# Optimization experiments

Measured on AMD Instinct MI355X. Metric: run time of the kernel, lower is better.

## Reference

```python
import jax, jax.numpy as jnp
import numpy as np

# Module hyperparameters (init_kwargs)
N_CODES = 1024    # context_size
Q_LEN = 8         # query_len
D_MODEL = 256     # d_model
BATCH = 16384
DECAY = 0.99
EPSILON = 1e-05


def setup_inputs() -> dict:
    key = jax.random.key(0)
    k1, k2, k3 = jax.random.split(key, 3)
    q = jax.random.normal(k1, (BATCH, Q_LEN, D_MODEL), jnp.float32)
    context = jax.random.normal(k2, (N_CODES, Q_LEN, D_MODEL), jnp.float32)
    ema_count = jnp.ones((N_CODES,), jnp.float32)
    ema_dw = jax.random.normal(k3, (N_CODES, Q_LEN, D_MODEL), jnp.float32) * 0.1
    return {"q": q, "context": context, "ema_count": ema_count, "ema_dw": ema_dw}


def _forward(q, context, ema_count, ema_dw):
    B, Q, D = q.shape
    N = context.shape[0]
    q_flat = q.reshape(B, Q * D)              # [B, QD]
    g_flat = context.reshape(N, Q * D)        # [N, QD]
    Dflat = Q * D

    # squared-euclidean cdist via the matmul expansion, then nearest code
    distances = (jnp.sum(q_flat * q_flat, axis=1, keepdims=True)
                 + jnp.sum(g_flat * g_flat, axis=1)
                 - 2.0 * (q_flat @ g_flat.T))                      # [B, N]
    indices = jnp.argmin(distances, axis=-1)                       # [B]

    # einsum('bn,nqd->bqd', one_hot, context) == gather
    q_context = context[indices]                                   # [B, Q, D]
    # einsum('bn,bqd->nqd', one_hot, q) == scatter-add by code id
    q_hat = jax.ops.segment_sum(q, indices, num_segments=N)        # [N, Q, D]

    # per-sample mean MSE (q_context detached in original)
    qld = jnp.mean((jax.lax.stop_gradient(q_context) - q) ** 2, axis=(1, 2))  # [B]

    # EMA codebook update (training mode, no-grad in original)
    counts = jax.ops.segment_sum(jnp.ones((B,), q.dtype), indices, num_segments=N)  # [N]
    ec = DECAY * ema_count + (1.0 - DECAY) * counts
    n = jnp.sum(ec)
    ec = (ec + EPSILON) / (n + Dflat * EPSILON) * n                # Laplace smoothing
    edw = DECAY * ema_dw + (1.0 - DECAY) * jax.lax.stop_gradient(q_hat)
    context_new = edw / ec[:, None, None]                          # [N, Q, D]

    # straight-through output uses the UPDATED (detached) context
    out_context = (q_hat + jax.lax.stop_gradient(context_new - q_hat)).reshape(-1, D)  # [N*Q, D]
    return qld, out_context, ec, edw, context_new


def reference(q, context, ema_count, ema_dw):
    return _forward(q, context, ema_count, ema_dw)
```

## Files before the change

kernel.cpp:

```cpp
#include <hip/hip_runtime.h>
#include <hip/hip_bf16.h>
#include <float.h>

#define BSZ 16384
#define NCODES 1024
#define QD 2048
#define NCHUNK 64
#define NCOLG 16

typedef _Float16 f16x8 __attribute__((ext_vector_type(8)));
typedef _Float16 f16x4 __attribute__((ext_vector_type(4)));
typedef float f32x4 __attribute__((ext_vector_type(4)));

static __device__ __forceinline__ float one_minus_decay() { return (float)(1.0 - 0.99); }

static __device__ __forceinline__ void async_copy16(const void* src, void* lds) {
    __builtin_amdgcn_global_load_lds((const __attribute__((address_space(1))) void*)src,
                                     (__attribute__((address_space(3))) void*)lds, 16, 0, 0);
}

__global__ void k_prep_all(const float* __restrict__ ctx, const float* __restrict__ q,
                           _Float16* __restrict__ gh, float* __restrict__ gsq,
                           _Float16* __restrict__ qh, float* __restrict__ qsq) {
    __shared__ float red[4];
    int tid = threadIdx.x;
    const float* src; _Float16* dh; float* nrm;
    if (blockIdx.x < NCODES) {
        size_t n = blockIdx.x;
        src = ctx + n * QD; dh = gh + n * QD; nrm = gsq + n;
    } else {
        size_t b = blockIdx.x - NCODES;
        src = q + b * QD; dh = qh + b * QD; nrm = qsq + b;
    }
    int c = tid * 8;
    float4 t0 = *(const float4*)(src + c);
    float4 t1 = *(const float4*)(src + c + 4);
    float s = t0.x * t0.x + t0.y * t0.y + t0.z * t0.z + t0.w * t0.w
            + t1.x * t1.x + t1.y * t1.y + t1.z * t1.z + t1.w * t1.w;
    f16x8 h;
    h[0] = (_Float16)t0.x; h[1] = (_Float16)t0.y;
    h[2] = (_Float16)t0.z; h[3] = (_Float16)t0.w;
    h[4] = (_Float16)t1.x; h[5] = (_Float16)t1.y;
    h[6] = (_Float16)t1.z; h[7] = (_Float16)t1.w;
    *(f16x8*)(dh + c) = h;
    for (int off = 32; off > 0; off >>= 1) s += __shfl_down(s, off);
    if ((tid & 63) == 0) red[tid >> 6] = s;
    __syncthreads();
    if (tid == 0) *nrm = red[0] + red[1] + red[2] + red[3];
}

__global__ void k_prep_r17(const float* __restrict__ ctx, const float* __restrict__ q,
                           _Float16* __restrict__ gh, float* __restrict__ gsq,
                           float* __restrict__ qsq) {
    int tid = threadIdx.x;
    if (blockIdx.x < NCODES) {
        __shared__ float red[4];
        int n = blockIdx.x;
        float s = 0.f;
#pragma unroll
        for (int i = 0; i < 2; ++i) {
            int c = (tid + i * 256) * 4;
            float4 t = *(const float4*)(ctx + (size_t)n * QD + c);
            f16x4 h;
            h[0] = (_Float16)t.x; h[1] = (_Float16)t.y;
            h[2] = (_Float16)t.z; h[3] = (_Float16)t.w;
            *(f16x4*)(gh + (size_t)n * QD + c) = h;
            s += t.x * t.x + t.y * t.y + t.z * t.z + t.w * t.w;
        }
        for (int off = 32; off > 0; off >>= 1) s += __shfl_down(s, off);
        if ((tid & 63) == 0) red[tid >> 6] = s;
        __syncthreads();
        if (tid == 0) gsq[n] = red[0] + red[1] + red[2] + red[3];
    } else {
        int w = tid >> 6, lane = tid & 63;
        int b = (blockIdx.x - NCODES) * 4 + w;
        const float4* row = (const float4*)(q + (size_t)b * QD);
        float s = 0.f;
#pragma unroll
        for (int i = 0; i < 8; ++i) {
            float4 v = row[lane + i * 64];
            s += v.x * v.x + v.y * v.y + v.z * v.z + v.w * v.w;
        }
        for (int off = 32; off > 0; off >>= 1) s += __shfl_down(s, off);
        if (lane == 0) qsq[b] = s;
    }
}

__launch_bounds__(256)
__global__ void k_dist_pre(const _Float16* __restrict__ qh, const _Float16* __restrict__ gh,
                           const float* __restrict__ gsq,
                           float* __restrict__ pval, int* __restrict__ pidx) {
    __shared__ _Float16 ah[128][64];
    __shared__ _Float16 bh[128][64];

    const int tid = threadIdx.x;
    const int lane = tid & 63, wid = tid >> 6;
    const int wr = wid >> 1, wc = wid & 1;
    const int n0 = blockIdx.x;
    const int xcd = n0 & 7, j = n0 >> 3;
    const int col = j & 7, rowt = xcd * 16 + (j >> 3);
    const int colBase = col * 128, rowBase = rowt * 128;
    const int fr = lane & 15, kg = lane >> 4;

    char* ahB = (char*)&ah[0][0];
    const char* bhB = (const char*)&bh[0][0];

    const int srow = lane >> 3;
    const int gran = (lane & 7) ^ (lane >> 3);

    f32x4 acc[4][4];
#pragma unroll
    for (int m = 0; m < 4; ++m)
#pragma unroll
        for (int n = 0; n < 4; ++n) acc[m][n] = (f32x4)0.f;

    for (int kb = 0; kb < QD; kb += 64) {
        __syncthreads();
#pragma unroll
        for (int i = 0; i < 4; ++i) {
            int g = wid * 4 + i;
            size_t aoff = (size_t)(rowBase + g * 8 + srow) * QD + kb + gran * 8;
            async_copy16(qh + aoff, &ah[g * 8][0]);
        }
#pragma unroll
        for (int i = 0; i < 4; ++i) {
            int g = wid * 4 + i;
            size_t goff = (size_t)(colBase + g * 8 + srow) * QD + kb + gran * 8;
            async_copy16(gh + goff, &bh[g * 8][0]);
        }
        __syncthreads();

#pragma unroll
        for (int h = 0; h < 2; ++h) {
            f16x8 a_h[4], b_h[4];
#pragma unroll
            for (int m = 0; m < 4; ++m) {
                int ar = wr * 64 + m * 16 + fr;
                int off = ar * 128 + ((h * 64 + kg * 16) ^ ((ar & 7) << 4));
                a_h[m] = *(const f16x8*)(ahB + off);
            }
#pragma unroll
            for (int n = 0; n < 4; ++n) {
                int br = wc * 64 + n * 16 + fr;
                int off = br * 128 + ((h * 64 + kg * 16) ^ ((br & 7) << 4));
                b_h[n] = *(const f16x8*)(bhB + off);
            }
#pragma unroll
            for (int m = 0; m < 4; ++m)
#pragma unroll
                for (int n = 0; n < 4; ++n)
                    acc[m][n] = __builtin_amdgcn_mfma_f32_16x16x32_f16(a_h[m], b_h[n], acc[m][n], 0, 0, 0);
        }
    }

    float mv[4][4]; int mi[4][4];
#pragma unroll
    for (int m = 0; m < 4; ++m)
#pragma unroll
        for (int r = 0; r < 4; ++r) { mv[m][r] = FLT_MAX; mi[m][r] = 0x7fffffff; }
#pragma unroll
    for (int n = 0; n < 4; ++n) {
        int c = colBase + wc * 64 + n * 16 + fr;
        float gq = gsq[c];
#pragma unroll
        for (int m = 0; m < 4; ++m)
#pragma unroll
            for (int r = 0; r < 4; ++r) {
                float d = gq - 2.0f * acc[m][n][r];
                if (d < mv[m][r]) { mv[m][r] = d; mi[m][r] = c; }
            }
    }
#pragma unroll
    for (int off = 1; off < 16; off <<= 1) {
#pragma unroll
        for (int m = 0; m < 4; ++m)
#pragma unroll
            for (int r = 0; r < 4; ++r) {
                float ov = __shfl_xor(mv[m][r], off);
                int   oi = __shfl_xor(mi[m][r], off);
                if (ov < mv[m][r] || (ov == mv[m][r] && oi < mi[m][r])) { mv[m][r] = ov; mi[m][r] = oi; }
            }
    }
    if (fr == 0) {
        const size_t slot = (size_t)(col * 2 + wc) * BSZ;
#pragma unroll
        for (int m = 0; m < 4; ++m)
#pragma unroll
            for (int r = 0; r < 4; ++r) {
                int grow = rowBase + wr * 64 + m * 16 + kg * 4 + r;
                pval[slot + grow] = mv[m][r];
                pidx[slot + grow] = mi[m][r];
            }
    }
}

__launch_bounds__(256)
__global__ void k_dist_r17(const float* __restrict__ q, const _Float16* __restrict__ gh,
                           const float* __restrict__ gsq,
                           float* __restrict__ pval, int* __restrict__ pidx) {
    __shared__ _Float16 ah[128][64];
    __shared__ _Float16 bh[128][64];

    const int tid = threadIdx.x;
    const int lane = tid & 63, wid = tid >> 6;
    const int wr = wid >> 1, wc = wid & 1;
    const int n0 = blockIdx.x;
    const int xcd = n0 & 7, j = n0 >> 3;
    const int col = j & 7, rowt = xcd * 16 + (j >> 3);
    const int colBase = col * 128, rowBase = rowt * 128;
    const int fr = lane & 15, kg = lane >> 4;

    char* ahB = (char*)&ah[0][0];
    const char* bhB = (const char*)&bh[0][0];

    f32x4 acc[4][4];
#pragma unroll
    for (int m = 0; m < 4; ++m)
#pragma unroll
        for (int n = 0; n < 4; ++n) acc[m][n] = (f32x4)0.f;

    for (int kb = 0; kb < QD; kb += 64) {
        __syncthreads();
#pragma unroll
        for (int s = 0; s < 8; ++s) {
            int f = s * 256 + tid;
            int row = f >> 4, k4 = (f & 15) * 4;
            float4 t = *(const float4*)(q + (size_t)(rowBase + row) * QD + kb + k4);
            f16x4 h;
            h[0] = (_Float16)t.x; h[1] = (_Float16)t.y;
            h[2] = (_Float16)t.z; h[3] = (_Float16)t.w;
            int byt = (row * 128 + k4 * 2) ^ ((row & 7) << 4);
            *(f16x4*)(ahB + byt) = h;
        }
#pragma unroll
        for (int i = 0; i < 4; ++i) {
            int g = wid * 4 + i;
            int row = g * 8 + (lane >> 3);
            int gran = (lane & 7) ^ (lane >> 3);
            size_t goff = (size_t)(colBase + row) * QD + kb + gran * 8;
            async_copy16(gh + goff, &bh[g * 8][0]);
        }
        __syncthreads();

#pragma unroll
        for (int h = 0; h < 2; ++h) {
            f16x8 a_h[4], b_h[4];
#pragma unroll
            for (int m = 0; m < 4; ++m) {
                int ar = wr * 64 + m * 16 + fr;
                int off = ar * 128 + ((h * 64 + kg * 16) ^ ((ar & 7) << 4));
                a_h[m] = *(const f16x8*)(ahB + off);
            }
#pragma unroll
            for (int n = 0; n < 4; ++n) {
                int br = wc * 64 + n * 16 + fr;
                int off = br * 128 + ((h * 64 + kg * 16) ^ ((br & 7) << 4));
                b_h[n] = *(const f16x8*)(bhB + off);
            }
#pragma unroll
            for (int m = 0; m < 4; ++m)
#pragma unroll
                for (int n = 0; n < 4; ++n)
                    acc[m][n] = __builtin_amdgcn_mfma_f32_16x16x32_f16(a_h[m], b_h[n], acc[m][n], 0, 0, 0);
        }
    }

    float mv[4][4]; int mi[4][4];
#pragma unroll
    for (int m = 0; m < 4; ++m)
#pragma unroll
        for (int r = 0; r < 4; ++r) { mv[m][r] = FLT_MAX; mi[m][r] = 0x7fffffff; }
#pragma unroll
    for (int n = 0; n < 4; ++n) {
        int c = colBase + wc * 64 + n * 16 + fr;
        float gq = gsq[c];
#pragma unroll
        for (int m = 0; m < 4; ++m)
#pragma unroll
            for (int r = 0; r < 4; ++r) {
                float d = gq - 2.0f * acc[m][n][r];
                if (d < mv[m][r]) { mv[m][r] = d; mi[m][r] = c; }
            }
    }
#pragma unroll
    for (int off = 1; off < 16; off <<= 1) {
#pragma unroll
        for (int m = 0; m < 4; ++m)
#pragma unroll
            for (int r = 0; r < 4; ++r) {
                float ov = __shfl_xor(mv[m][r], off);
                int   oi = __shfl_xor(mi[m][r], off);
                if (ov < mv[m][r] || (ov == mv[m][r] && oi < mi[m][r])) { mv[m][r] = ov; mi[m][r] = oi; }
            }
    }
    if (fr == 0) {
        const size_t slot = (size_t)(col * 2 + wc) * BSZ;
#pragma unroll
        for (int m = 0; m < 4; ++m)
#pragma unroll
            for (int r = 0; r < 4; ++r) {
                int grow = rowBase + wr * 64 + m * 16 + kg * 4 + r;
                pval[slot + grow] = mv[m][r];
                pidx[slot + grow] = mi[m][r];
            }
    }
}

__global__ void k_merge(const float* __restrict__ pval, const int* __restrict__ pidx,
                        const float* __restrict__ qsq,
                        int* __restrict__ idx_out, float* __restrict__ qld,
                        int* __restrict__ chunkhist) {
    __shared__ int h[NCODES];
    int c = blockIdx.x, tid = threadIdx.x;
    int b = c * 256 + tid;
#pragma unroll
    for (int s = 0; s < 4; ++s) h[tid + s * 256] = 0;
    float bv = pval[b]; int bi = pidx[b];
    for (int y = 1; y < NCOLG; ++y) {
        float v = pval[(size_t)y * BSZ + b]; int ii = pidx[(size_t)y * BSZ + b];
        if (v < bv || (v == bv && ii < bi)) { bv = v; bi = ii; }
    }
    idx_out[b] = bi;
    qld[b] = (qsq[b] + bv) * (1.0f / (float)QD);
    __syncthreads();
    atomicAdd(&h[bi], 1);
    __syncthreads();
#pragma unroll
    for (int s = 0; s < 4; ++s) chunkhist[c * NCODES + tid + s * 256] = h[tid + s * 256];
}

__global__ void k_scan(const int* __restrict__ chunkhist, int* __restrict__ base,
                       int* __restrict__ counts, int* __restrict__ offsets,
                       const float* __restrict__ ema_count, float* __restrict__ ec_out) {
    __shared__ int s[NCODES];
    __shared__ float e2[NCODES];
    int code = threadIdx.x;
    int run = 0;
    for (int c = 0; c < NCHUNK; ++c) {
        base[c * NCODES + code] = run;
        run += chunkhist[c * NCODES + code];
    }
    counts[code] = run;
    s[code] = run; __syncthreads();
    for (int off = 1; off < NCODES; off <<= 1) {
        int v = (code >= off) ? s[code - off] : 0;
        __syncthreads();
        s[code] += v; __syncthreads();
    }
    offsets[code] = s[code] - run;
    float er = 0.99f * ema_count[code] + one_minus_decay() * (float)run;
    e2[code] = er; __syncthreads();
    for (int off = 512; off > 0; off >>= 1) {
        if (code < off) e2[code] += e2[code + off];
        __syncthreads();
    }
    float n = e2[0];
    ec_out[code] = (er + 1e-5f) / (n + (float)(2048.0 * 1e-5)) * n;
}

__global__ void k_fill(const int* __restrict__ idx, const int* __restrict__ base,
                       const int* __restrict__ offsets, int* __restrict__ list) {
    __shared__ int sidx[256];
    int c = blockIdx.x, tid = threadIdx.x;
    int b = c * 256 + tid;
    int n = idx[b];
    sidx[tid] = n; __syncthreads();
    int rank = 0;
    for (int j = 0; j < tid; ++j) rank += (sidx[j] == n);
    list[offsets[n] + base[c * NCODES + n] + rank] = b;
}

__global__ void k_qhat(const float* __restrict__ q, const int* __restrict__ counts,
                       const int* __restrict__ offsets, const int* __restrict__ list,
                       float* __restrict__ qhat) {
    int n = blockIdx.x;
    int col = blockIdx.y * 256 + threadIdx.x;
    int cnt = counts[n];
    const int* lp = list + offsets[n];
    float a0 = 0.f, a1 = 0.f, a2 = 0.f, a3 = 0.f, a4 = 0.f, a5 = 0.f, a6 = 0.f, a7 = 0.f;
    int i = 0;
    for (; i + 8 <= cnt; i += 8) {
        int b0 = lp[i], b1 = lp[i + 1], b2 = lp[i + 2], b3 = lp[i + 3];
        int b4 = lp[i + 4], b5 = lp[i + 5], b6 = lp[i + 6], b7 = lp[i + 7];
        a0 += q[(size_t)b0 * QD + col]; a1 += q[(size_t)b1 * QD + col];
        a2 += q[(size_t)b2 * QD + col]; a3 += q[(size_t)b3 * QD + col];
        a4 += q[(size_t)b4 * QD + col]; a5 += q[(size_t)b5 * QD + col];
        a6 += q[(size_t)b6 * QD + col]; a7 += q[(size_t)b7 * QD + col];
    }
    for (; i < cnt; ++i) a0 += q[(size_t)lp[i] * QD + col];
    float r = ((a0 + a1) + (a2 + a3)) + ((a4 + a5) + (a6 + a7));
    qhat[(size_t)n * QD + col] = r;
}

__global__ void k_fin(const float* __restrict__ ema_dw, const float* __restrict__ ec,
                      const float* qhat, float* edw_out, float* ctxnew_out,
                      float* outctx_out) {
    size_t i = ((size_t)blockIdx.x * 256 + threadIdx.x) * 8;
    int n = (int)(i >> 11);
    float e = ec[n];
    float om = one_minus_decay();
#pragma unroll
    for (int h = 0; h < 2; ++h) {
        float4 dw = *(const float4*)(ema_dw + i + h * 4);
        float4 qh = *(const float4*)(qhat + i + h * 4);
        float4 ed, cn;
        ed.x = 0.99f * dw.x + om * qh.x; ed.y = 0.99f * dw.y + om * qh.y;
        ed.z = 0.99f * dw.z + om * qh.z; ed.w = 0.99f * dw.w + om * qh.w;
        cn.x = ed.x / e; cn.y = ed.y / e; cn.z = ed.z / e; cn.w = ed.w / e;
        *(float4*)(edw_out + i + h * 4) = ed;
        *(float4*)(ctxnew_out + i + h * 4) = cn;
        *(float4*)(outctx_out + i + h * 4) = cn;
    }
}

extern "C" void kernel_launch(void* const* d_in, const int* in_sizes, int n_in,
                              void* d_out, int out_size, void* d_ws, size_t ws_size,
                              hipStream_t stream) {
    const float* q         = (const float*)d_in[0];
    const float* ctx       = (const float*)d_in[1];
    const float* ema_count = (const float*)d_in[2];
    const float* ema_dw    = (const float*)d_in[3];

    float* out = (float*)d_out;
    float* o_qld    = out;
    float* o_outctx = out + BSZ;
    float* o_ec     = o_outctx + (size_t)NCODES * QD;
    float* o_edw    = o_ec + NCODES;
    float* o_ctxnew = o_edw + (size_t)NCODES * QD;

    char* w = (char*)d_ws;
    float* ws_gsq   = (float*)w;
    int* ws_idx     = (int*)(w + 4096);
    int* ws_counts  = (int*)(w + 4096 + 65536);
    int* ws_offsets = ws_counts + NCODES;
    int* ws_list    = ws_offsets + NCODES;

    const size_t presplit_need = (size_t)1048576 + (size_t)BSZ * QD * sizeof(_Float16);
    const bool use_pre = (ws_size >= presplit_need);
    _Float16* qh = (_Float16*)(w + 1048576);

    _Float16* gh = (_Float16*)o_ctxnew;
    float* pval  = o_edw;
    int*   pidx  = (int*)(o_edw + (size_t)NCOLG * BSZ);
    float* qsq   = o_edw + (size_t)2 * NCOLG * BSZ;
    int* chunkhist = (int*)o_outctx;
    int* basep     = chunkhist + NCHUNK * NCODES;
    float* qhat    = o_outctx;

    if (use_pre) {
        k_prep_all<<<NCODES + BSZ, 256, 0, stream>>>(ctx, q, gh, ws_gsq, qh, qsq);
        k_dist_pre<<<1024, 256, 0, stream>>>(qh, gh, ws_gsq, pval, pidx);
    } else {
        k_prep_r17<<<NCODES + BSZ / 4, 256, 0, stream>>>(ctx, q, gh, ws_gsq, qsq);
        k_dist_r17<<<1024, 256, 0, stream>>>(q, gh, ws_gsq, pval, pidx);
    }
    k_merge <<<NCHUNK, 256, 0, stream>>>(pval, pidx, qsq, ws_idx, o_qld, chunkhist);
    k_scan  <<<1, 1024, 0, stream>>>(chunkhist, basep, ws_counts, ws_offsets, ema_count, o_ec);
    k_fill  <<<NCHUNK, 256, 0, stream>>>(ws_idx, basep, ws_offsets, ws_list);
    k_qhat  <<<dim3(NCODES, 8), 256, 0, stream>>>(q, ws_counts, ws_offsets, ws_list, qhat);
    k_fin   <<<NCODES * QD / 2048, 256, 0, stream>>>(ema_dw, o_ec, qhat,
                                                     o_edw, o_ctxnew, o_outctx);
}
```

Before: 212.4 us.

## Double K-step per sync in distance GEMM and gather q_hat from fp16 copy

The distance GEMM now loads two 64-wide K slices into doubled LDS buffers per barrier pair, halving the number of sync points and issuing more async loads at once. The q_hat segment sum now reads the fp16 copy of q instead of fp32, halving gather bandwidth. The cost is twice the LDS per block, which may reduce occupancy, and fp16 rounding of q in the q_hat sums, which lowers accuracy.

Result: faster. 200.9 us (-5.4%).

```diff
diff --git a/kernel.cpp b/kernel.cpp
--- a/kernel.cpp
+++ b/kernel.cpp
@@ -90,8 +90,8 @@
 __global__ void k_dist_pre(const _Float16* __restrict__ qh, const _Float16* __restrict__ gh,
                            const float* __restrict__ gsq,
                            float* __restrict__ pval, int* __restrict__ pidx) {
-    __shared__ _Float16 ah[128][64];
-    __shared__ _Float16 bh[128][64];
+    __shared__ _Float16 ah[2][128][64];
+    __shared__ _Float16 bh[2][128][64];
 
     const int tid = threadIdx.x;
     const int lane = tid & 63, wid = tid >> 6;
@@ -102,9 +102,6 @@
     const int colBase = col * 128, rowBase = rowt * 128;
     const int fr = lane & 15, kg = lane >> 4;
 
-    char* ahB = (char*)&ah[0][0];
-    const char* bhB = (const char*)&bh[0][0];
-
     const int srow = lane >> 3;
     const int gran = (lane & 7) ^ (lane >> 3);
 
@@ -114,42 +111,46 @@
 #pragma unroll
         for (int n = 0; n < 4; ++n) acc[m][n] = (f32x4)0.f;
 
-    for (int kb = 0; kb < QD; kb += 64) {
-        __syncthreads();
-#pragma unroll
-        for (int i = 0; i < 4; ++i) {
-            int g = wid * 4 + i;
-            size_t aoff = (size_t)(rowBase + g * 8 + srow) * QD + kb + gran * 8;
-            async_copy16(qh + aoff, &ah[g * 8][0]);
-        }
-#pragma unroll
-        for (int i = 0; i < 4; ++i) {
-            int g = wid * 4 + i;
-            size_t goff = (size_t)(colBase + g * 8 + srow) * QD + kb + gran * 8;
-            async_copy16(gh + goff, &bh[g * 8][0]);
-        }
-        __syncthreads();
-
-#pragma unroll
-        for (int h = 0; h < 2; ++h) {
-            f16x8 a_h[4], b_h[4];
-#pragma unroll
-            for (int m = 0; m < 4; ++m) {
-                int ar = wr * 64 + m * 16 + fr;
-                int off = ar * 128 + ((h * 64 + kg * 16) ^ ((ar & 7) << 4));
-                a_h[m] = *(const f16x8*)(ahB + off);
-            }
-#pragma unroll
-            for (int n = 0; n < 4; ++n) {
-                int br = wc * 64 + n * 16 + fr;
-                int off = br * 128 + ((h * 64 + kg * 16) ^ ((br & 7) << 4));
-                b_h[n] = *(const f16x8*)(bhB + off);
-            }
-#pragma unroll
-            for (int m = 0; m < 4; ++m)
-#pragma unroll
-                for (int n = 0; n < 4; ++n)
-                    acc[m][n] = __builtin_amdgcn_mfma_f32_16x16x32_f16(a_h[m], b_h[n], acc[m][n], 0, 0, 0);
+    for (int kb = 0; kb < QD; kb += 128) {
+        __syncthreads();
+#pragma unroll
+        for (int d = 0; d < 2; ++d) {
+#pragma unroll
+            for (int i = 0; i < 4; ++i) {
+                int g = wid * 4 + i;
+                size_t roff = (size_t)(rowBase + g * 8 + srow) * QD + kb + d * 64 + gran * 8;
+                size_t coff = (size_t)(colBase + g * 8 + srow) * QD + kb + d * 64 + gran * 8;
+                async_copy16(qh + roff, &ah[d][g * 8][0]);
+                async_copy16(gh + coff, &bh[d][g * 8][0]);
+            }
+        }
+        __syncthreads();
+
+#pragma unroll
+        for (int d = 0; d < 2; ++d) {
+            const char* ahB = (const char*)&ah[d][0][0];
+            const char* bhB = (const char*)&bh[d][0][0];
+#pragma unroll
+            for (int h = 0; h < 2; ++h) {
+                f16x8 a_h[4], b_h[4];
+#pragma unroll
+                for (int m = 0; m < 4; ++m) {
+                    int ar = wr * 64 + m * 16 + fr;
+                    int off = ar * 128 + ((h * 64 + kg * 16) ^ ((ar & 7) << 4));
+                    a_h[m] = *(const f16x8*)(ahB + off);
+                }
+#pragma unroll
+                for (int n = 0; n < 4; ++n) {
+                    int br = wc * 64 + n * 16 + fr;
+                    int off = br * 128 + ((h * 64 + kg * 16) ^ ((br & 7) << 4));
+                    b_h[n] = *(const f16x8*)(bhB + off);
+                }
+#pragma unroll
+                for (int m = 0; m < 4; ++m)
+#pragma unroll
+                    for (int n = 0; n < 4; ++n)
+                        acc[m][n] = __builtin_amdgcn_mfma_f32_16x16x32_f16(a_h[m], b_h[n], acc[m][n], 0, 0, 0);
+            }
         }
     }
 
@@ -370,9 +371,31 @@
     list[offsets[n] + base[c * NCODES + n] + rank] = b;
 }
 
-__global__ void k_qhat(const float* __restrict__ q, const int* __restrict__ counts,
-                       const int* __restrict__ offsets, const int* __restrict__ list,
-                       float* __restrict__ qhat) {
+__global__ void k_qhat_h(const _Float16* __restrict__ qh, const int* __restrict__ counts,
+                         const int* __restrict__ offsets, const int* __restrict__ list,
+                         float* __restrict__ qhat) {
+    int n = blockIdx.x;
+    int col = blockIdx.y * 256 + threadIdx.x;
+    int cnt = counts[n];
+    const int* lp = list + offsets[n];
+    float a0 = 0.f, a1 = 0.f, a2 = 0.f, a3 = 0.f, a4 = 0.f, a5 = 0.f, a6 = 0.f, a7 = 0.f;
+    int i = 0;
+    for (; i + 8 <= cnt; i += 8) {
+        int b0 = lp[i], b1 = lp[i + 1], b2 = lp[i + 2], b3 = lp[i + 3];
+        int b4 = lp[i + 4], b5 = lp[i + 5], b6 = lp[i + 6], b7 = lp[i + 7];
+        a0 += (float)qh[(size_t)b0 * QD + col]; a1 += (float)qh[(size_t)b1 * QD + col];
+        a2 += (float)qh[(size_t)b2 * QD + col]; a3 += (float)qh[(size_t)b3 * QD + col];
+        a4 += (float)qh[(size_t)b4 * QD + col]; a5 += (float)qh[(size_t)b5 * QD + col];
+        a6 += (float)qh[(size_t)b6 * QD + col]; a7 += (float)qh[(size_t)b7 * QD + col];
+    }
+    for (; i < cnt; ++i) a0 += (float)qh[(size_t)lp[i] * QD + col];
+    float r = ((a0 + a1) + (a2 + a3)) + ((a4 + a5) + (a6 + a7));
+    qhat[(size_t)n * QD + col] = r;
+}
+
+__global__ void k_qhat_f(const float* __restrict__ q, const int* __restrict__ counts,
+                         const int* __restrict__ offsets, const int* __restrict__ list,
+                         float* __restrict__ qhat) {
     int n = blockIdx.x;
     int col = blockIdx.y * 256 + threadIdx.x;
     int cnt = counts[n];
@@ -457,7 +480,11 @@
     k_merge <<<NCHUNK, 256, 0, stream>>>(pval, pidx, qsq, ws_idx, o_qld, chunkhist);
     k_scan  <<<1, 1024, 0, stream>>>(chunkhist, basep, ws_counts, ws_offsets, ema_count, o_ec);
     k_fill  <<<NCHUNK, 256, 0, stream>>>(ws_idx, basep, ws_offsets, ws_list);
-    k_qhat  <<<dim3(NCODES, 8), 256, 0, stream>>>(q, ws_counts, ws_offsets, ws_list, qhat);
+    if (use_pre) {
+        k_qhat_h<<<dim3(NCODES, 8), 256, 0, stream>>>(qh, ws_counts, ws_offsets, ws_list, qhat);
+    } else {
+        k_qhat_f<<<dim3(NCODES, 8), 256, 0, stream>>>(q, ws_counts, ws_offsets, ws_list, qhat);
+    }
     k_fin   <<<NCODES * QD / 2048, 256, 0, stream>>>(ema_dw, o_ec, qhat,
                                                      o_edw, o_ctxnew, o_outctx);
 }
```
